# Performance work log

Hardware: AMD Instinct MI355X
Metric: run time of the kernel (lower is better)

## Reference

```python
import jax, jax.numpy as jnp
import numpy as np

BOUND = 1.0
MIN_NEAR = 0.05
NUM_STEPS = 64
UP_STEPS = 64
DENSITY_SCALE = 1.0
N_RAYS = 16384
HIDDEN = 64


def setup_inputs() -> dict:
    key = jax.random.key(0)
    ks = jax.random.split(key, 8)
    # cameras hover near z=2 looking roughly toward -z so rays hit the [-1,1]^3 AABB
    rays_o = jax.random.normal(ks[0], (N_RAYS, 3), jnp.float32) * 0.1 + jnp.array([0.0, 0.0, 2.0])
    rays_d = jax.random.normal(ks[1], (N_RAYS, 3), jnp.float32) * 0.2 + jnp.array([0.0, 0.0, -1.0])
    rays_d = rays_d / jnp.linalg.norm(rays_d, axis=-1, keepdims=True)
    W1 = jax.random.normal(ks[2], (3, HIDDEN), jnp.float32) / jnp.sqrt(3.0)
    b1 = jnp.zeros((HIDDEN,), jnp.float32)
    w_sigma = jax.random.normal(ks[3], (HIDDEN, 1), jnp.float32) / jnp.sqrt(float(HIDDEN))
    b_sigma = jnp.zeros((1,), jnp.float32)
    W_rgb = jax.random.normal(ks[4], (HIDDEN, 3), jnp.float32) / jnp.sqrt(float(HIDDEN))
    b_rgb = jnp.zeros((3,), jnp.float32)
    return {"rays_o": rays_o, "rays_d": rays_d, "W1": W1, "b1": b1,
            "w_sigma": w_sigma, "b_sigma": b_sigma, "W_rgb": W_rgb, "b_rgb": b_rgb}


def near_far_cube(rays_o, rays_d, bound, min_near):
    tmin = (-bound - rays_o) / (rays_d + 1e-15)
    tmax = (bound - rays_o) / (rays_d + 1e-15)
    near = jnp.max(jnp.minimum(tmin, tmax), axis=-1, keepdims=True)
    far = jnp.min(jnp.maximum(tmin, tmax), axis=-1, keepdims=True)
    miss = far < near
    near = jnp.where(miss, 1e9, near)
    far = jnp.where(miss, 1e9, far)
    near = jnp.maximum(near, min_near)
    return near, far


def sample_pdf(bins, weights, n_samples):
    # bins: [N, M+1], weights: [N, M]; deterministic (det=True) inverse-CDF sampling
    weights = weights + 1e-5
    pdf = weights / jnp.sum(weights, -1, keepdims=True)
    cdf = jnp.cumsum(pdf, -1)
    cdf = jnp.concatenate([jnp.zeros_like(cdf[..., :1]), cdf], -1)  # [N, M+1]
    u = jnp.linspace(0.5 / n_samples, 1.0 - 0.5 / n_samples, n_samples, dtype=cdf.dtype)
    u = jnp.broadcast_to(u, cdf.shape[:-1] + (n_samples,))
    inds = jax.vmap(lambda c, uu: jnp.searchsorted(c, uu, side='right'))(cdf, u)
    below = jnp.maximum(inds - 1, 0)
    above = jnp.minimum(inds, cdf.shape[-1] - 1)
    cdf_b = jnp.take_along_axis(cdf, below, -1)
    cdf_a = jnp.take_along_axis(cdf, above, -1)
    bins_b = jnp.take_along_axis(bins, below, -1)
    bins_a = jnp.take_along_axis(bins, above, -1)
    denom = cdf_a - cdf_b
    denom = jnp.where(denom < 1e-5, jnp.ones_like(denom), denom)
    t = (u - cdf_b) / denom
    return bins_b + t * (bins_a - bins_b)


def mlp(pts, W1, b1, w_sigma, b_sigma, W_rgb, b_rgb):
    h = jax.nn.relu(pts @ W1 + b1)                      # [N, T, HIDDEN]
    sigma = jax.nn.softplus(h @ w_sigma + b_sigma)[..., 0]  # [N, T]
    rgb = jax.nn.sigmoid(h @ W_rgb + b_rgb)             # [N, T, 3]
    return sigma, rgb


def alpha_composite_weights(z_vals, sigma, sample_dist):
    deltas = z_vals[..., 1:] - z_vals[..., :-1]
    deltas = jnp.concatenate([deltas, jnp.broadcast_to(sample_dist, deltas[..., :1].shape)], -1)
    alphas = 1.0 - jnp.exp(-deltas * DENSITY_SCALE * sigma)
    trans = jnp.cumprod(jnp.concatenate([jnp.ones_like(alphas[..., :1]), 1.0 - alphas + 1e-15], -1)[..., :-1], -1)
    return alphas * trans


def reference(rays_o, rays_d, W1, b1, w_sigma, b_sigma, W_rgb, b_rgb):
    rays_d = rays_d / jnp.linalg.norm(rays_d, axis=-1, keepdims=True)
    near, far = near_far_cube(rays_o, rays_d, BOUND, MIN_NEAR)  # [N,1]
    sample_dist = (far - near) / NUM_STEPS                      # [N,1]

    # coarse stratified (deterministic) samples
    z = jnp.linspace(0.0, 1.0, NUM_STEPS, dtype=rays_o.dtype)
    z_vals = near + (far - near) * z                            # [N,T]
    xyzs = rays_o[:, None, :] + rays_d[:, None, :] * z_vals[..., None]
    xyzs = jnp.clip(xyzs, -BOUND, BOUND)
    sigma, _ = mlp(xyzs, W1, b1, w_sigma, b_sigma, W_rgb, b_rgb)
    weights = alpha_composite_weights(z_vals, sigma, sample_dist)

    # inverse-CDF importance resampling (no-grad in original)
    z_mid = 0.5 * (z_vals[..., :-1] + z_vals[..., 1:])          # [N,T-1]
    new_z = sample_pdf(z_mid, weights[:, 1:-1], UP_STEPS)       # [N,UP]
    new_z = jax.lax.stop_gradient(new_z)

    z_all = jnp.sort(jnp.concatenate([z_vals, new_z], -1), -1)  # [N,T+UP]
    xyzs_all = rays_o[:, None, :] + rays_d[:, None, :] * z_all[..., None]
    xyzs_all = jnp.clip(xyzs_all, -BOUND, BOUND)
    sigma_all, rgb_all = mlp(xyzs_all, W1, b1, w_sigma, b_sigma, W_rgb, b_rgb)
    weights_all = alpha_composite_weights(z_all, sigma_all, sample_dist)

    weights_sum = jnp.sum(weights_all, -1)                      # [N]
    image = jnp.sum(weights_all[..., None] * rgb_all, axis=-2)  # [N,3]
    image = image + (1.0 - weights_sum)[..., None]              # white background
    return image
```

## Files before the change

kernel.cpp:

```cpp
#include <hip/hip_runtime.h>
#include <math.h>

#define WAVES_PER_BLOCK 4

typedef float v2f __attribute__((ext_vector_type(2)));
typedef float v4f __attribute__((ext_vector_type(4)));

__device__ __forceinline__ float fast_rcp(float x) { return __builtin_amdgcn_rcpf(x); }

#define DPP_ROW_SHR(n)  (0x110 | (n))
#define DPP_WF_SL1      0x130
#define DPP_WF_SR1      0x138
#define DPP_ROW_BCAST15 0x142
#define DPP_ROW_BCAST31 0x143

template <int CTRL, int RM = 0xf, int BM = 0xf, bool BC = false>
__device__ __forceinline__ float fdpp(float old_, float src) {
    return __int_as_float(__builtin_amdgcn_update_dpp(
        __float_as_int(old_), __float_as_int(src), CTRL, RM, BM, BC));
}

__device__ __forceinline__ float lane63_bcast(float x) {
    return __int_as_float(__builtin_amdgcn_readlane(__float_as_int(x), 63));
}
__device__ __forceinline__ float rdlane(float x, int l) {
    return __int_as_float(__builtin_amdgcn_readlane(__float_as_int(x), l));
}

__device__ __forceinline__ float scan_add_dpp(float x) {
    x += fdpp<DPP_ROW_SHR(1)>(0.0f, x);
    x += fdpp<DPP_ROW_SHR(2)>(0.0f, x);
    x += fdpp<DPP_ROW_SHR(4)>(0.0f, x);
    x += fdpp<DPP_ROW_SHR(8)>(0.0f, x);
    x += fdpp<DPP_ROW_BCAST15, 0xa>(0.0f, x);
    x += fdpp<DPP_ROW_BCAST31, 0xc>(0.0f, x);
    return x;
}
__device__ __forceinline__ float scan_mul_dpp(float x) {
    x *= fdpp<DPP_ROW_SHR(1)>(1.0f, x);
    x *= fdpp<DPP_ROW_SHR(2)>(1.0f, x);
    x *= fdpp<DPP_ROW_SHR(4)>(1.0f, x);
    x *= fdpp<DPP_ROW_SHR(8)>(1.0f, x);
    x *= fdpp<DPP_ROW_BCAST15, 0xa>(1.0f, x);
    x *= fdpp<DPP_ROW_BCAST31, 0xc>(1.0f, x);
    return x;
}
__device__ __forceinline__ float wave_sum_dpp(float x) {
    return lane63_bcast(scan_add_dpp(x));
}

__device__ __forceinline__ float softplus_f(float x) {
    return fmaxf(x, 0.0f) + __logf(1.0f + __expf(-fabsf(x)));
}
__device__ __forceinline__ float sigmoid_f(float x) {
    return fast_rcp(1.0f + __expf(-x));
}
__device__ __forceinline__ float clamp1(float x) {
    return fminf(fmaxf(x, -1.0f), 1.0f);
}

template <bool LE>
__device__ __forceinline__ int rank2(const float* a, float own, float x) {
    int o = 0;
#pragma unroll
    for (int t = 0; t < 8; ++t) {
        float p = rdlane(own, 8 * t + 7);
        o += (int)(LE ? (p <= x) : (p < x));
    }
    o = (o < 7) ? o : 7;
    const v4f q0 = *(const v4f*)&a[8 * o];
    const v4f q1 = *(const v4f*)&a[8 * o + 4];
    int cnt = 0;
    cnt += (int)(LE ? (q0.x <= x) : (q0.x < x));
    cnt += (int)(LE ? (q0.y <= x) : (q0.y < x));
    cnt += (int)(LE ? (q0.z <= x) : (q0.z < x));
    cnt += (int)(LE ? (q0.w <= x) : (q0.w < x));
    cnt += (int)(LE ? (q1.x <= x) : (q1.x < x));
    cnt += (int)(LE ? (q1.y <= x) : (q1.y < x));
    cnt += (int)(LE ? (q1.z <= x) : (q1.z < x));
    cnt += (int)(LE ? (q1.w <= x) : (q1.w < x));
    return 8 * o + cnt;
}

__global__ __launch_bounds__(WAVES_PER_BLOCK * 64)
void nerf_render_kernel(const float* __restrict__ rays_o,
                        const float* __restrict__ rays_d,
                        const float* __restrict__ W1,
                        const float* __restrict__ b1,
                        const float* __restrict__ w_sigma,
                        const float* __restrict__ b_sigma,
                        const float* __restrict__ W_rgb,
                        const float* __restrict__ b_rgb,
                        float* __restrict__ out)
{
    const int tid  = threadIdx.x;
    const int lane = tid & 63;
    const int wv   = tid >> 6;
    const int ray  = __builtin_amdgcn_readfirstlane(blockIdx.x * WAVES_PER_BLOCK + wv);

    __shared__ __align__(16) float s_pref[WAVES_PER_BLOCK][65][8];
    __shared__ __align__(16) float s_kne [WAVES_PER_BLOCK][64];
    __shared__ __align__(16) float s_zmid[WAVES_PER_BLOCK][64];
    __shared__ __align__(16) float s_cdf [WAVES_PER_BLOCK][64];
    __shared__ __align__(16) float s_zall[WAVES_PER_BLOCK][128];

    float ox = rays_o[ray * 3 + 0], oy = rays_o[ray * 3 + 1], oz = rays_o[ray * 3 + 2];
    float dx = rays_d[ray * 3 + 0], dy = rays_d[ray * 3 + 1], dz = rays_d[ray * 3 + 2];
    {
        float inv = __builtin_amdgcn_rsqf(dx * dx + dy * dy + dz * dz);
        dx *= inv; dy *= inv; dz *= inv;
    }

    float rx = fast_rcp(dx + 1e-15f);
    float ry = fast_rcp(dy + 1e-15f);
    float rz = fast_rcp(dz + 1e-15f);
    float t0x = (-1.0f - ox) * rx, t1x = (1.0f - ox) * rx;
    float t0y = (-1.0f - oy) * ry, t1y = (1.0f - oy) * ry;
    float t0z = (-1.0f - oz) * rz, t1z = (1.0f - oz) * rz;
    float nearv = fmaxf(fmaxf(fminf(t0x, t1x), fminf(t0y, t1y)), fminf(t0z, t1z));
    float farv  = fminf(fminf(fmaxf(t0x, t1x), fmaxf(t0y, t1y)), fmaxf(t0z, t1z));
    const bool miss = (farv < nearv);
    if (miss) { nearv = 1e9f; farv = 1e9f; }
    nearv = fmaxf(nearv, 0.05f);
    const float sample_dist = (farv - nearv) * (1.0f / 64.0f);

    const float wS = w_sigma[lane];
    const float wR = W_rgb[3 * lane + 0];
    const float wG = W_rgb[3 * lane + 1];
    const float wB = W_rgb[3 * lane + 2];

    float cj, mj;
    {
        float w1x = W1[lane], w1y = W1[64 + lane], w1z = W1[128 + lane];
        float eox = ox, eoy = oy, eoz = oz, msc = 1.0f;
        if (miss) {
            eox = clamp1(fmaf(dx, 1e9f, ox));
            eoy = clamp1(fmaf(dy, 1e9f, oy));
            eoz = clamp1(fmaf(dz, 1e9f, oz));
            msc = 0.0f;
        }
        cj = fmaf(eox, w1x, fmaf(eoy, w1y, fmaf(eoz, w1z, b1[lane])));
        mj = msc * fmaf(dx, w1x, fmaf(dy, w1y, dz * w1z));
    }

    const bool m0 = (mj == 0.0f);
    const bool mneg = (mj < 0.0f);
    float knee = m0 ? 3e38f : (-cj * fast_rcp(mj));
    float t  = m0 ? 0.0f : (mneg ? -1.0f : 1.0f);
    float tm = t * mj, tc = t * cj;
    float pc = mneg ? cj : (m0 ? fmaxf(cj, 0.0f) : 0.0f);
    float qc = mneg ? mj : 0.0f;

    unsigned kb  = __float_as_uint(knee);
    unsigned ord = kb ^ ((kb & 0x80000000u) ? 0xFFFFFFFFu : 0x80000000u);
    unsigned key = (ord & ~63u) | (unsigned)lane;

    float* keyU = s_zmid[wv];
    float* kneeS = s_kne[wv];
    keyU[lane] = __uint_as_float(key);

    int p = 0;
#pragma unroll
    for (int g = 0; g < 16; ++g) {
        v4f q = *(const v4f*)&keyU[4 * g];
        p += (int)(__float_as_uint(q.x) < key);
        p += (int)(__float_as_uint(q.y) < key);
        p += (int)(__float_as_uint(q.z) < key);
        p += (int)(__float_as_uint(q.w) < key);
    }
    kneeS[p] = knee;
    *(v4f*)&s_pref[wv][p][0] = (v4f){wS * tm, wS * tc, wR * tm, wR * tc};
    *(v4f*)&s_pref[wv][p][4] = (v4f){wG * tm, wG * tc, wB * tm, wB * tc};

    const float bs0 = b_sigma[0];
    float QpS = wave_sum_dpp(wS * qc), PpS = wave_sum_dpp(wS * pc) + bs0;
    float QpR = wave_sum_dpp(wR * qc), PpR = wave_sum_dpp(wR * pc) + b_rgb[0];
    float QpG = wave_sum_dpp(wG * qc), PpG = wave_sum_dpp(wG * pc) + b_rgb[1];
    float QpB = wave_sum_dpp(wB * qc), PpB = wave_sum_dpp(wB * pc) + b_rgb[2];

    v4f d0 = *(const v4f*)&s_pref[wv][lane][0];
    v4f d1 = *(const v4f*)&s_pref[wv][lane][4];
    float own_knee = kneeS[lane];

    float iAs = scan_add_dpp(d0.x) + QpS, iBs = scan_add_dpp(d0.y) + PpS;
    float iAr = scan_add_dpp(d0.z) + QpR, iBr = scan_add_dpp(d0.w) + PpR;
    float iAg = scan_add_dpp(d1.x) + QpG, iBg = scan_add_dpp(d1.y) + PpG;
    float iAb = scan_add_dpp(d1.z) + QpB, iBb = scan_add_dpp(d1.w) + PpB;

    *(v4f*)&s_pref[wv][lane + 1][0] = (v4f){iAs, iBs, iAr, iBr};
    *(v4f*)&s_pref[wv][lane + 1][4] = (v4f){iAg, iBg, iAb, iBb};
    if (lane == 0) {
        *(v4f*)&s_pref[wv][0][0] = (v4f){QpS, PpS, QpR, PpR};
        *(v4f*)&s_pref[wv][0][4] = (v4f){QpG, PpG, QpB, PpB};
    }

    float z = nearv + (farv - nearv) * ((float)lane * (1.0f / 63.0f));
    float sigma;
    {
        int k = rank2<false>(kneeS, own_knee, z);
        v2f ab = *(const v2f*)&s_pref[wv][k][0];
        sigma = softplus_f(fmaf(ab.x, z, ab.y));
    }

    float z_next = fdpp<DPP_WF_SL1>(0.0f, z);
    float delta  = (lane < 63) ? (z_next - z) : sample_dist;
    float alpha  = 1.0f - __expf(-delta * sigma);
    float v      = 1.0f - alpha + 1e-15f;
    float incl   = scan_mul_dpp(v);
    float trans  = fdpp<DPP_WF_SR1>(1.0f, incl);
    float w = alpha * trans;

    float wgt = (lane >= 1 && lane <= 62) ? (w + 1e-5f) : 0.0f;
    float cumw = scan_add_dpp(wgt);
    float total = lane63_bcast(cumw);
    float cdf_incl = cumw * fast_rcp(total);

    float zmid = 0.5f * (z + z_next);
    float cdfv = (lane < 63) ? cdf_incl : 2.0f;
    s_zmid[wv][lane] = (lane < 63) ? zmid : 0.0f;
    s_cdf [wv][lane] = cdfv;

    float u = 0.0078125f + (float)lane * 0.015625f;
    int ind = rank2<true>(s_cdf[wv], cdfv, u);
    int below = ind - 1;
    int above = (ind < 62) ? ind : 62;
    float cb = s_cdf[wv][below], ca = s_cdf[wv][above];
    float bb = s_zmid[wv][below], ba = s_zmid[wv][above];
    float denom = ca - cb;
    if (denom < 1e-5f) denom = 1.0f;
    float tt = (u - cb) * fast_rcp(denom);
    float nz = fmaf(tt, ba - bb, bb);

    s_zmid[wv][lane] = z;
    s_cdf [wv][lane] = nz;
    int pa  = lane + rank2<false>(s_cdf [wv], nz, z);
    int pb2 = lane + rank2<true >(s_zmid[wv], z,  nz);
    s_zall[wv][pa]  = z;
    s_zall[wv][pb2] = nz;

    v2f za = *(const v2f*)&s_zall[wv][2 * lane];
    float za0 = za.x;
    float za1 = za.y;

    int k0 = rank2<false>(kneeS, own_knee, za0);
    int k1 = rank2<false>(kneeS, own_knee, za1);
    v4f A0 = *(const v4f*)&s_pref[wv][k0][0];
    v4f A1 = *(const v4f*)&s_pref[wv][k0][4];
    v4f B0 = *(const v4f*)&s_pref[wv][k1][0];
    v4f B1 = *(const v4f*)&s_pref[wv][k1][4];

    float sg0 = softplus_f(fmaf(A0.x, za0, A0.y));
    float r0  = sigmoid_f (fmaf(A0.z, za0, A0.w));
    float g0  = sigmoid_f (fmaf(A1.x, za0, A1.y));
    float bl0 = sigmoid_f (fmaf(A1.z, za0, A1.w));
    float sg1 = softplus_f(fmaf(B0.x, za1, B0.y));
    float r1  = sigmoid_f (fmaf(B0.z, za1, B0.w));
    float g1  = sigmoid_f (fmaf(B1.x, za1, B1.y));
    float bl1 = sigmoid_f (fmaf(B1.z, za1, B1.w));

    float zn0 = fdpp<DPP_WF_SL1>(0.0f, za0);
    float d0f = za1 - za0;
    float d1f = (lane < 63) ? (zn0 - za1) : sample_dist;
    float a0 = 1.0f - __expf(-d0f * sg0);
    float a1 = 1.0f - __expf(-d1f * sg1);
    float v0 = 1.0f - a0 + 1e-15f;
    float v1 = 1.0f - a1 + 1e-15f;
    float local = v0 * v1;
    float incl2 = scan_mul_dpp(local);
    float eprod = fdpp<DPP_WF_SR1>(1.0f, incl2);
    float w0 = a0 * eprod;
    float w1 = a1 * (eprod * v0);

    float wsum = wave_sum_dpp(w0 + w1);
    float rs   = wave_sum_dpp(fmaf(w0, r0,  w1 * r1));
    float gs   = wave_sum_dpp(fmaf(w0, g0,  w1 * g1));
    float bs   = wave_sum_dpp(fmaf(w0, bl0, w1 * bl1));

    if (lane == 0) {
        float bg = 1.0f - wsum;
        out[ray * 3 + 0] = rs + bg;
        out[ray * 3 + 1] = gs + bg;
        out[ray * 3 + 2] = bs + bg;
    }
}

extern "C" void kernel_launch(void* const* d_in, const int* in_sizes, int n_in,
                              void* d_out, int out_size, void* d_ws, size_t ws_size,
                              hipStream_t stream) {
    const float* rays_o  = (const float*)d_in[0];
    const float* rays_d  = (const float*)d_in[1];
    const float* W1      = (const float*)d_in[2];
    const float* b1      = (const float*)d_in[3];
    const float* w_sigma = (const float*)d_in[4];
    const float* b_sigma = (const float*)d_in[5];
    const float* W_rgb   = (const float*)d_in[6];
    const float* b_rgb   = (const float*)d_in[7];
    float* out = (float*)d_out;

    const int n_rays = in_sizes[0] / 3;
    dim3 grid((n_rays + WAVES_PER_BLOCK - 1) / WAVES_PER_BLOCK);
    dim3 block(WAVES_PER_BLOCK * 64);
    hipLaunchKernelGGL(nerf_render_kernel, grid, block, 0, stream,
                       rays_o, rays_d, W1, b1, w_sigma, b_sigma, W_rgb, b_rgb, out);
}
```

Measured before the change: 91.14 us.

## Replace knee sorting with scatter-add of knee contributions into sample bins

Drops the per-wave sort of the 64 ReLU knees and the per-sample rank search over the sorted knees. Each hidden unit now finds which sample interval its knee falls into and atomically adds its slope and intercept terms into that bin. A prefix scan over the bins then gives the piecewise-linear MLP coefficients at every sample. Shared memory is merged into a single per-wave arena. The cost is LDS atomics and zero-initialisation passes, and summing floats in atomic order may change the results slightly.

```diff
diff --git a/kernel.cpp b/kernel.cpp
--- a/kernel.cpp
+++ b/kernel.cpp
@@ -81,6 +81,14 @@
     cnt += (int)(LE ? (q1.w <= x) : (q1.w < x));
     return 8 * o + cnt;
 }
+
+#define FT_OFF   0
+#define CT_OFF   0
+#define ZARR_OFF 132
+#define ZMID_OFF 196
+#define NZ_OFF   1056
+#define ZALL_OFF 1120
+#define ARENA_F  1248
 
 __global__ __launch_bounds__(WAVES_PER_BLOCK * 64)
 void nerf_render_kernel(const float* __restrict__ rays_o,
@@ -98,11 +106,14 @@
     const int wv   = tid >> 6;
     const int ray  = __builtin_amdgcn_readfirstlane(blockIdx.x * WAVES_PER_BLOCK + wv);
 
-    __shared__ __align__(16) float s_pref[WAVES_PER_BLOCK][65][8];
-    __shared__ __align__(16) float s_kne [WAVES_PER_BLOCK][64];
-    __shared__ __align__(16) float s_zmid[WAVES_PER_BLOCK][64];
-    __shared__ __align__(16) float s_cdf [WAVES_PER_BLOCK][64];
-    __shared__ __align__(16) float s_zall[WAVES_PER_BLOCK][128];
+    __shared__ __align__(16) float s_arena[WAVES_PER_BLOCK][ARENA_F];
+    float* const AR    = s_arena[wv];
+    float* const CT    = AR + CT_OFF;
+    float* const zarr  = AR + ZARR_OFF;
+    float* const zmid  = AR + ZMID_OFF;
+    float* const FT    = AR + FT_OFF;
+    float* const nzarr = AR + NZ_OFF;
+    float* const zall  = AR + ZALL_OFF;
 
     float ox = rays_o[ray * 3 + 0], oy = rays_o[ray * 3 + 1], oz = rays_o[ray * 3 + 2];
     float dx = rays_d[ray * 3 + 0], dy = rays_d[ray * 3 + 1], dz = rays_d[ray * 3 + 2];
@@ -148,29 +159,8 @@
     float knee = m0 ? 3e38f : (-cj * fast_rcp(mj));
     float t  = m0 ? 0.0f : (mneg ? -1.0f : 1.0f);
     float tm = t * mj, tc = t * cj;
+    float qc = mneg ? mj : 0.0f;
     float pc = mneg ? cj : (m0 ? fmaxf(cj, 0.0f) : 0.0f);
-    float qc = mneg ? mj : 0.0f;
-
-    unsigned kb  = __float_as_uint(knee);
-    unsigned ord = kb ^ ((kb & 0x80000000u) ? 0xFFFFFFFFu : 0x80000000u);
-    unsigned key = (ord & ~63u) | (unsigned)lane;
-
-    float* keyU = s_zmid[wv];
-    float* kneeS = s_kne[wv];
-    keyU[lane] = __uint_as_float(key);
-
-    int p = 0;
-#pragma unroll
-    for (int g = 0; g < 16; ++g) {
-        v4f q = *(const v4f*)&keyU[4 * g];
-        p += (int)(__float_as_uint(q.x) < key);
-        p += (int)(__float_as_uint(q.y) < key);
-        p += (int)(__float_as_uint(q.z) < key);
-        p += (int)(__float_as_uint(q.w) < key);
-    }
-    kneeS[p] = knee;
-    *(v4f*)&s_pref[wv][p][0] = (v4f){wS * tm, wS * tc, wR * tm, wR * tc};
-    *(v4f*)&s_pref[wv][p][4] = (v4f){wG * tm, wG * tc, wB * tm, wB * tc};
 
     const float bs0 = b_sigma[0];
     float QpS = wave_sum_dpp(wS * qc), PpS = wave_sum_dpp(wS * pc) + bs0;
@@ -178,29 +168,19 @@
     float QpG = wave_sum_dpp(wG * qc), PpG = wave_sum_dpp(wG * pc) + b_rgb[1];
     float QpB = wave_sum_dpp(wB * qc), PpB = wave_sum_dpp(wB * pc) + b_rgb[2];
 
-    v4f d0 = *(const v4f*)&s_pref[wv][lane][0];
-    v4f d1 = *(const v4f*)&s_pref[wv][lane][4];
-    float own_knee = kneeS[lane];
-
-    float iAs = scan_add_dpp(d0.x) + QpS, iBs = scan_add_dpp(d0.y) + PpS;
-    float iAr = scan_add_dpp(d0.z) + QpR, iBr = scan_add_dpp(d0.w) + PpR;
-    float iAg = scan_add_dpp(d1.x) + QpG, iBg = scan_add_dpp(d1.y) + PpG;
-    float iAb = scan_add_dpp(d1.z) + QpB, iBb = scan_add_dpp(d1.w) + PpB;
-
-    *(v4f*)&s_pref[wv][lane + 1][0] = (v4f){iAs, iBs, iAr, iBr};
-    *(v4f*)&s_pref[wv][lane + 1][4] = (v4f){iAg, iBg, iAb, iBb};
-    if (lane == 0) {
-        *(v4f*)&s_pref[wv][0][0] = (v4f){QpS, PpS, QpR, PpR};
-        *(v4f*)&s_pref[wv][0][4] = (v4f){QpG, PpG, QpB, PpB};
-    }
-
     float z = nearv + (farv - nearv) * ((float)lane * (1.0f / 63.0f));
-    float sigma;
-    {
-        int k = rank2<false>(kneeS, own_knee, z);
-        v2f ab = *(const v2f*)&s_pref[wv][k][0];
-        sigma = softplus_f(fmaf(ab.x, z, ab.y));
-    }
+    zarr[lane] = z;
+    *(v2f*)&CT[2 * lane] = (v2f){0.0f, 0.0f};
+    if (lane == 0) *(v2f*)&CT[128] = (v2f){0.0f, 0.0f};
+
+    int ej = rank2<true>(zarr, z, knee);
+    atomicAdd(&CT[2 * ej + 0], wS * tm);
+    atomicAdd(&CT[2 * ej + 1], wS * tc);
+
+    v2f ct = *(const v2f*)&CT[2 * lane];
+    float SA = scan_add_dpp(ct.x);
+    float SB = scan_add_dpp(ct.y);
+    float sigma = softplus_f(fmaf(QpS + SA, z, PpS + SB));
 
     float z_next = fdpp<DPP_WF_SL1>(0.0f, z);
     float delta  = (lane < 63) ? (z_next - z) : sample_dist;
@@ -215,48 +195,78 @@
     float total = lane63_bcast(cumw);
     float cdf_incl = cumw * fast_rcp(total);
 
-    float zmid = 0.5f * (z + z_next);
     float cdfv = (lane < 63) ? cdf_incl : 2.0f;
-    s_zmid[wv][lane] = (lane < 63) ? zmid : 0.0f;
-    s_cdf [wv][lane] = cdfv;
+    zmid [lane] = 0.5f * (z + z_next);
+    nzarr[lane] = cdfv;
 
     float u = 0.0078125f + (float)lane * 0.015625f;
-    int ind = rank2<true>(s_cdf[wv], cdfv, u);
+    int ind = rank2<true>(nzarr, cdfv, u);
     int below = ind - 1;
     int above = (ind < 62) ? ind : 62;
-    float cb = s_cdf[wv][below], ca = s_cdf[wv][above];
-    float bb = s_zmid[wv][below], ba = s_zmid[wv][above];
+    float cb = nzarr[below], ca = nzarr[above];
+    float bb = zmid [below], ba = zmid [above];
     float denom = ca - cb;
     if (denom < 1e-5f) denom = 1.0f;
     float tt = (u - cb) * fast_rcp(denom);
     float nz = fmaf(tt, ba - bb, bb);
 
-    s_zmid[wv][lane] = z;
-    s_cdf [wv][lane] = nz;
-    int pa  = lane + rank2<false>(s_cdf [wv], nz, z);
-    int pb2 = lane + rank2<true >(s_zmid[wv], z,  nz);
-    s_zall[wv][pa]  = z;
-    s_zall[wv][pb2] = nz;
-
-    v2f za = *(const v2f*)&s_zall[wv][2 * lane];
+    nzarr[lane] = nz;
+    int pa  = lane + rank2<false>(nzarr, nz, z);
+    int pb2 = lane + rank2<true >(zarr,  z,  nz);
+    zall[pa]  = z;
+    zall[pb2] = nz;
+
+    v2f za = *(const v2f*)&zall[2 * lane];
     float za0 = za.x;
     float za1 = za.y;
 
-    int k0 = rank2<false>(kneeS, own_knee, za0);
-    int k1 = rank2<false>(kneeS, own_knee, za1);
-    v4f A0 = *(const v4f*)&s_pref[wv][k0][0];
-    v4f A1 = *(const v4f*)&s_pref[wv][k0][4];
-    v4f B0 = *(const v4f*)&s_pref[wv][k1][0];
-    v4f B1 = *(const v4f*)&s_pref[wv][k1][4];
-
-    float sg0 = softplus_f(fmaf(A0.x, za0, A0.y));
-    float r0  = sigmoid_f (fmaf(A0.z, za0, A0.w));
-    float g0  = sigmoid_f (fmaf(A1.x, za0, A1.y));
-    float bl0 = sigmoid_f (fmaf(A1.z, za0, A1.w));
-    float sg1 = softplus_f(fmaf(B0.x, za1, B0.y));
-    float r1  = sigmoid_f (fmaf(B0.z, za1, B0.w));
-    float g1  = sigmoid_f (fmaf(B1.x, za1, B1.y));
-    float bl1 = sigmoid_f (fmaf(B1.z, za1, B1.w));
+    int fj = rank2<true>(nzarr, nz, knee);
+    int ep = ej + fj;
+
+#pragma unroll
+    for (int ch = 0; ch < 8; ++ch) {
+        *(v2f*)&FT[132 * ch + 2 * lane] = (v2f){0.0f, 0.0f};
+    }
+    if (lane == 0) {
+#pragma unroll
+        for (int ch = 0; ch < 8; ++ch) FT[132 * ch + 128] = 0.0f;
+    }
+    atomicAdd(&FT[132 * 0 + ep], wS * tm);
+    atomicAdd(&FT[132 * 1 + ep], wS * tc);
+    atomicAdd(&FT[132 * 2 + ep], wR * tm);
+    atomicAdd(&FT[132 * 3 + ep], wR * tc);
+    atomicAdd(&FT[132 * 4 + ep], wG * tm);
+    atomicAdd(&FT[132 * 5 + ep], wG * tc);
+    atomicAdd(&FT[132 * 6 + ep], wB * tm);
+    atomicAdd(&FT[132 * 7 + ep], wB * tc);
+
+    v2f bS = *(const v2f*)&FT[132 * 0 + 2 * lane];
+    v2f cS = *(const v2f*)&FT[132 * 1 + 2 * lane];
+    v2f bR = *(const v2f*)&FT[132 * 2 + 2 * lane];
+    v2f cR = *(const v2f*)&FT[132 * 3 + 2 * lane];
+    v2f bG = *(const v2f*)&FT[132 * 4 + 2 * lane];
+    v2f cG = *(const v2f*)&FT[132 * 5 + 2 * lane];
+    v2f bb2 = *(const v2f*)&FT[132 * 6 + 2 * lane];
+    v2f cB = *(const v2f*)&FT[132 * 7 + 2 * lane];
+
+    float s1S = scan_add_dpp(bS.x + bS.y), s1Sc = scan_add_dpp(cS.x + cS.y);
+    float s1R = scan_add_dpp(bR.x + bR.y), s1Rc = scan_add_dpp(cR.x + cR.y);
+    float s1G = scan_add_dpp(bG.x + bG.y), s1Gc = scan_add_dpp(cG.x + cG.y);
+    float s1B = scan_add_dpp(bb2.x + bb2.y), s1Bc = scan_add_dpp(cB.x + cB.y);
+
+    float preS1 = fmaf(QpS + s1S, za1, PpS + s1Sc);
+    float preR1 = fmaf(QpR + s1R, za1, PpR + s1Rc);
+    float preG1 = fmaf(QpG + s1G, za1, PpG + s1Gc);
+    float preB1 = fmaf(QpB + s1B, za1, PpB + s1Bc);
+    float preS0 = fmaf(QpS + (s1S - bS.y), za0, PpS + (s1Sc - cS.y));
+    float preR0 = fmaf(QpR + (s1R - bR.y), za0, PpR + (s1Rc - cR.y));
+    float preG0 = fmaf(QpG + (s1G - bG.y), za0, PpG + (s1Gc - cG.y));
+    float preB0 = fmaf(QpB + (s1B - bb2.y), za0, PpB + (s1Bc - cB.y));
+
+    float sg0 = softplus_f(preS0), sg1 = softplus_f(preS1);
+    float r0  = sigmoid_f (preR0), r1  = sigmoid_f (preR1);
+    float g0  = sigmoid_f (preG0), g1  = sigmoid_f (preG1);
+    float bl0 = sigmoid_f (preB0), bl1 = sigmoid_f (preB1);
 
     float zn0 = fdpp<DPP_WF_SL1>(0.0f, za0);
     float d0f = za1 - za0;
```

Measured after the change: 127.4 us. +39.8%, slower.
